# Performance work log

Measured on AMD Instinct MI355X. Metric: run time of the kernel, lower is better.

The kernel has to match this reference:

```python
import jax, jax.numpy as jnp
import numpy as np

C = 256
H = 8          # num_heads
G = 8          # groupnorm groups
EPS = 1e-6     # attention eps
GN_EPS = 1e-5  # torch GroupNorm default eps


def setup_inputs() -> dict:
    key = jax.random.key(0)
    ks = jax.random.split(key, 8)
    s = 1.0 / np.sqrt(C)
    return {
        "x": jax.random.normal(ks[0], (2, C, 32, 32, 32), dtype=jnp.float32),
        "gn_gamma": jnp.ones((C,), dtype=jnp.float32),
        "gn_beta": jnp.zeros((C,), dtype=jnp.float32),
        "wq": jax.random.normal(ks[1], (C, C), dtype=jnp.float32) * s,
        "wk": jax.random.normal(ks[2], (C, C), dtype=jnp.float32) * s,
        "wv": jax.random.normal(ks[3], (C, C), dtype=jnp.float32) * s,
        "w_out": jax.random.normal(ks[4], (C, C), dtype=jnp.float32) * s,
        "b_out": jnp.zeros((C,), dtype=jnp.float32),
    }


def reference(x, gn_gamma, gn_beta, wq, wk, wv, w_out, b_out):
    B, Cc, X, Y, Z = x.shape
    N = X * Y * Z
    D = Cc // H  # head_dim

    xf = x.reshape(B, Cc, N)

    # GroupNorm over (C/G, N) per group
    xg = xf.reshape(B, G, (Cc // G) * N)
    mean = jnp.mean(xg, axis=-1, keepdims=True)
    var = jnp.var(xg, axis=-1, keepdims=True)
    xn = ((xg - mean) * jax.lax.rsqrt(var + GN_EPS)).reshape(B, Cc, N)
    xn = xn * gn_gamma[None, :, None] + gn_beta[None, :, None]

    # 1x1x1 conv projections == channel matmuls
    q = jnp.einsum('oc,bcn->bon', wq, xn).reshape(B, H, D, N)
    k = jnp.einsum('oc,bcn->bon', wk, xn).reshape(B, H, D, N)
    v = jnp.einsum('oc,bcn->bon', wv, xn).reshape(B, H, D, N)

    qm = jax.nn.elu(q) + 1.0  # [B,H,D,N]
    km = jax.nn.elu(k) + 1.0

    # context: sum_j phi(k)_j v_j^T  -> [B,H,D,D]
    context = jnp.einsum('bhdn,bhen->bhde', km, v)
    # numerator: context @ phi(q)  -> [B,H,D,N] (axis d contracts with phi(q)'s feature dim)
    numerator = jnp.einsum('bhde,bhdn->bhen', context, qm)
    # denominator per token
    k_sum = jnp.sum(km, axis=-1)  # [B,H,D]
    denom = jnp.einsum('bhdn,bhd->bhn', qm, k_sum)  # [B,H,N]

    out = numerator / (denom[:, :, None, :] + EPS)  # [B,H,D,N]
    out = out.reshape(B, Cc, N)

    out = jnp.einsum('oc,bcn->bon', w_out, out) + b_out[None, :, None]
    out = out.reshape(B, Cc, X, Y, Z)
    return out + x
```

## Files before the change

### kernel.cpp

```cpp
#include <hip/hip_runtime.h>
#include <math.h>

#define BB 2
#define CC 256
#define NHEAD 8
#define HD 32
#define NGRP 8
#define NNTOK 32768
#define ATT_EPS 1e-6f
#define GN_EPS 1e-5f

typedef __attribute__((ext_vector_type(8))) short bfrag8;
typedef __attribute__((ext_vector_type(4))) float accf4;

__device__ __forceinline__ float b2f(unsigned short u) {
    unsigned int x = ((unsigned int)u) << 16;
    return __uint_as_float(x);
}
__device__ __forceinline__ unsigned short f2b(float f) {
    unsigned int x = __float_as_uint(f);
    unsigned int r = x + 0x7fffu + ((x >> 16) & 1u);
    return (unsigned short)(r >> 16);
}
__device__ __forceinline__ void gl_lds16(const void* g, void* s) {
    __builtin_amdgcn_global_load_lds(
        (const __attribute__((address_space(1))) unsigned int*)g,
        (__attribute__((address_space(3))) unsigned int*)s, 16, 0, 0);
}

#define WS_QMT   0ull
#define WS_XNT   (WS_QMT + 8388608ull)
#define WS_WSTOLD (WS_XNT + 8650752ull)
#define WS_PART  (WS_WSTOLD + 101632ull)
#define WS_CTX2  WS_PART
#define WS_GNP2  (WS_PART + 32768ull)
#define WS_WST2  (WS_PART + 65536ull)
#define WS_BIAS  (WS_PART + 262144ull)
#define WS_GNPO  (WS_PART + 4325376ull)
#define WS_SCALE (WS_GNPO + 2048ull)
#define WS_SHIFT (WS_SCALE + 512ull)
#define WS_CTXO  (WS_SHIFT + 512ull)
#define WS_KSUM  (WS_CTXO + 16384ull)
#define WS_AMAT  (WS_KSUM + 512ull)

#define LDS_QS_OFF  17408
#define LDS_KSP_OFF 27648
#define LDS_BIAS_OFF 49152
#define LDS_QKV_TOTAL 49664

__global__ __launch_bounds__(256) void xn_gn(const float* __restrict__ x,
                                             unsigned short* __restrict__ xn_t,
                                             float* __restrict__ gnp2) {
    __shared__ unsigned short xt[64][264];
    __shared__ float ls[64];
    int b = blockIdx.y, n0 = blockIdx.x * 64, t = threadIdx.x;
    int col4 = (t & 15) * 4;
    float gs[8], gs2[8];
    #pragma unroll
    for (int g = 0; g < 8; ++g) { gs[g] = 0.f; gs2[g] = 0.f; }
    #pragma unroll
    for (int i = 0; i < 16; ++i) {
        int c = (t >> 4) + i * 16;
        const float4 v = *(const float4*)(x + (size_t)(b * CC + c) * NNTOK + n0 + col4);
        gs[i >> 1]  += v.x + v.y + v.z + v.w;
        gs2[i >> 1] += v.x * v.x + v.y * v.y + v.z * v.z + v.w * v.w;
        xt[col4 + 0][c] = f2b(v.x);
        xt[col4 + 1][c] = f2b(v.y);
        xt[col4 + 2][c] = f2b(v.z);
        xt[col4 + 3][c] = f2b(v.w);
    }
    int lane = t & 63, w = t >> 6;
    #pragma unroll
    for (int g = 0; g < 8; ++g) {
        float a = gs[g], a2 = gs2[g];
        #pragma unroll
        for (int off = 32; off; off >>= 1) {
            a  += __shfl_down(a, off);
            a2 += __shfl_down(a2, off);
        }
        if (lane == 0) { ls[w * 16 + g * 2] = a; ls[w * 16 + g * 2 + 1] = a2; }
    }
    __syncthreads();
    if (t < 16)
        gnp2[(size_t)(b * 512 + blockIdx.x) * 16 + t] =
            ls[t] + ls[16 + t] + ls[32 + t] + ls[48 + t];
    int n = t >> 2, q = t & 3;
    const char* src = (const char*)&xt[n][0] + q * 128;
    char* dst = (char*)(xn_t + ((size_t)b * NNTOK + n0 + n) * 264) + q * 128;
    #pragma unroll
    for (int i = 0; i < 8; ++i)
        *(float4*)(dst + i * 16) = *(const float4*)(src + i * 16);
}

__global__ __launch_bounds__(256) void gn_stats2(const float* __restrict__ gnp2,
                                                 const float* __restrict__ gamma,
                                                 const float* __restrict__ beta,
                                                 float* __restrict__ scale,
                                                 float* __restrict__ shift,
                                                 float* __restrict__ ctx2) {
    __shared__ float red[256];
    __shared__ float mean_l[16], rstd_l[16];
    int t = threadIdx.x;
    for (int i = t; i < 16 * 1056; i += 256) ctx2[i] = 0.f;
    int combo = t >> 3, sl = t & 7;
    int b2 = combo >> 4, idx = combo & 15;
    float a = 0.f;
    for (int k = sl; k < 512; k += 8)
        a += gnp2[(size_t)(b2 * 512 + k) * 16 + idx];
    red[t] = a;
    __syncthreads();
    if (t < 32) {
        float s = 0.f;
        #pragma unroll
        for (int j = 0; j < 8; ++j) s += red[t * 8 + j];
        red[t] = s;
    }
    __syncthreads();
    if (t < 16) {
        const float inv = 1.0f / (float)((CC / NGRP) * NNTOK);
        float m = red[t * 2] * inv;
        float var = red[t * 2 + 1] * inv - m * m;
        mean_l[t] = m;
        rstd_l[t] = rsqrtf(var + GN_EPS);
    }
    __syncthreads();
    for (int i = t; i < BB * CC; i += 256) {
        int b = i >> 8, c = i & 255;
        int g = b * 8 + (c >> 5);
        float sc = gamma[c] * rstd_l[g];
        scale[i] = sc;
        shift[i] = beta[c] - mean_l[g] * sc;
    }
}

__global__ __launch_bounds__(256) void fold_w(const float* __restrict__ wq,
                                              const float* __restrict__ wk,
                                              const float* __restrict__ wv,
                                              const float* __restrict__ scale,
                                              const float* __restrict__ shift,
                                              unsigned short* __restrict__ Wst2,
                                              float* __restrict__ bias) {
    int slice = blockIdx.x, h = blockIdx.y, b2 = blockIdx.z, t = threadIdx.x;
    __shared__ float sc_l[256], sh_l[256];
    sc_l[t] = scale[b2 * CC + t];
    sh_l[t] = shift[b2 * CC + t];
    __syncthreads();
    const float* Ws[3] = {wq, wk, wv};
    unsigned short* wdst = Wst2 + (size_t)(b2 * NHEAD + h) * 24576;
    for (int i = slice * 3072 + t; i < (slice + 1) * 3072; i += 256) {
        int e = i & 7;
        int chunk = i >> 3;
        int lane = chunk & 63;
        int kcmi = chunk >> 6;
        int mi = kcmi % 6;
        int kc = kcmi / 6;
        int lr = lane & 15, lq = lane >> 4;
        int row = mi * 16 + lr;
        int col = kc * 32 + lq * 8 + e;
        float v = Ws[row >> 5][(size_t)(h * 32 + (row & 31)) * CC + col] * sc_l[col];
        wdst[i] = f2b(v);
    }
    if (t < 96) {
        int rl = t >> 3, sub = t & 7;
        int r = slice * 12 + rl;
        const float* wrow = Ws[r >> 5] + (size_t)(h * 32 + (r & 31)) * CC + sub * 32;
        float sp = 0.f;
        #pragma unroll
        for (int k = 0; k < 8; ++k) {
            const float4 v4 = *(const float4*)(wrow + k * 4);
            const float* shp = &sh_l[sub * 32 + k * 4];
            sp += v4.x * shp[0] + v4.y * shp[1] + v4.z * shp[2] + v4.w * shp[3];
        }
        sp += __shfl_xor(sp, 1);
        sp += __shfl_xor(sp, 2);
        sp += __shfl_xor(sp, 4);
        if (sub == 0) bias[(size_t)(b2 * NHEAD + h) * 96 + r] = sp;
    }
}

__global__ __launch_bounds__(256, 3) void qkv_ctx(
    const unsigned short* __restrict__ xn_t, const unsigned short* __restrict__ Wst2,
    const float* __restrict__ bias,
    unsigned short* __restrict__ qm_t, float* __restrict__ ctx2) {
    __shared__ char lds[LDS_QKV_TOTAL];
    const int id = blockIdx.x;
    const int xcd = id & 7;
    const int j = id >> 3;
    const int h = j & 7;
    const int rem = j >> 3;
    const int tile = xcd * 32 + (rem & 31);
    const int b = rem >> 5;
    const int t = threadIdx.x;
    const int lane = t & 63, w = t >> 6;
    const int lr = lane & 15, lq = lane >> 4;
    const int n0 = tile * 128;

    {
        const char* wg = (const char*)(Wst2 + (size_t)(b * NHEAD + h) * 24576);
        for (int jj = w; jj < 48; jj += 4)
            gl_lds16(wg + jj * 1024 + lane * 16, lds + jj * 1024);
        if (t < 96)
            ((float*)(lds + LDS_BIAS_OFF))[t] = bias[(size_t)(b * NHEAD + h) * 96 + t];
    }
    __syncthreads();

    accf4 acc[6][2];
    #pragma unroll
    for (int i = 0; i < 6; ++i)
        #pragma unroll
        for (int jj = 0; jj < 2; ++jj) acc[i][jj] = (accf4){0.f, 0.f, 0.f, 0.f};

    const unsigned short* xr0 = xn_t + ((size_t)b * NNTOK + n0 + w * 32 + lr) * 264 + lq * 8;
    const unsigned short* xr1 = xr0 + 16 * 264;
    const char* wl = lds;

    bfrag8 wnx[6], bnx[2];
    #pragma unroll
    for (int mi = 0; mi < 6; ++mi)
        wnx[mi] = *(const bfrag8*)(wl + (0 * 6 + mi) * 1024 + lane * 16);
    bnx[0] = *(const bfrag8*)xr0;
    bnx[1] = *(const bfrag8*)xr1;

    #pragma unroll
    for (int kc = 0; kc < 8; ++kc) {
        bfrag8 wcur[6];
        #pragma unroll
        for (int mi = 0; mi < 6; ++mi) wcur[mi] = wnx[mi];
        bfrag8 bcur[2] = {bnx[0], bnx[1]};
        if (kc < 7) {
            #pragma unroll
            for (int mi = 0; mi < 6; ++mi)
                wnx[mi] = *(const bfrag8*)(wl + ((kc + 1) * 6 + mi) * 1024 + lane * 16);
            bnx[0] = *(const bfrag8*)(xr0 + (kc + 1) * 32);
            bnx[1] = *(const bfrag8*)(xr1 + (kc + 1) * 32);
        }
        #pragma unroll
        for (int mi = 0; mi < 6; ++mi)
            #pragma unroll
            for (int ci = 0; ci < 2; ++ci)
                acc[mi][ci] = __builtin_amdgcn_mfma_f32_16x16x32_bf16(wcur[mi], bcur[ci], acc[mi][ci], 0, 0, 0);
    }
    __syncthreads();

    const float* biasl = (const float*)(lds + LDS_BIAS_OFF);
    char* kmv = lds;
    char* qs  = lds + LDS_QS_OFF;
    #pragma unroll
    for (int mi = 0; mi < 2; ++mi)
        #pragma unroll
        for (int ci = 0; ci < 2; ++ci)
            #pragma unroll
            for (int r = 0; r < 4; ++r) {
                int d = mi * 16 + lq * 4 + r;
                int n = w * 32 + ci * 16 + lr;
                float q = acc[mi][ci][r] + biasl[d];
                *(unsigned short*)(qs + n * 80 + d * 2) = f2b(q > 0.f ? q + 1.f : __expf(q));
            }
    #pragma unroll
    for (int mi = 2; mi < 4; ++mi)
        #pragma unroll
        for (int ci = 0; ci < 2; ++ci)
            #pragma unroll
            for (int r = 0; r < 4; ++r) {
                int d = (mi - 2) * 16 + lq * 4 + r;
                int n = w * 32 + ci * 16 + lr;
                float kk = acc[mi][ci][r] + biasl[32 + d];
                *(unsigned short*)(kmv + d * 272 + n * 2) = f2b(kk > 0.f ? kk + 1.f : __expf(kk));
            }
    #pragma unroll
    for (int mi = 4; mi < 6; ++mi)
        #pragma unroll
        for (int ci = 0; ci < 2; ++ci)
            #pragma unroll
            for (int r = 0; r < 4; ++r) {
                int e = (mi - 4) * 16 + lq * 4 + r;
                int n = w * 32 + ci * 16 + lr;
                *(unsigned short*)(kmv + (32 + e) * 272 + n * 2) = f2b(acc[mi][ci][r] + biasl[64 + e]);
            }
    __syncthreads();

    float* ctx2p = ctx2 + (size_t)(b * NHEAD + h) * 1056;

    {
        char* qg = (char*)(qm_t + ((size_t)(b * NHEAD + h) * NNTOK + n0) * 32);
        int n = t >> 1, half = t & 1;
        const char* src = qs + n * 80 + half * 32;
        char* dst = qg + n * 64 + half * 32;
        *(float4*)dst = *(const float4*)src;
        *(float4*)(dst + 16) = *(const float4*)(src + 16);
    }

    {
        int qr = w >> 1, qc = w & 1;
        accf4 cacc = (accf4){0.f, 0.f, 0.f, 0.f};
        #pragma unroll
        for (int kk = 0; kk < 4; ++kk) {
            bfrag8 a  = *(const bfrag8*)(kmv + (qr * 16 + lr) * 272 + kk * 64 + lq * 16);
            bfrag8 bb = *(const bfrag8*)(kmv + (32 + qc * 16 + lr) * 272 + kk * 64 + lq * 16);
            cacc = __builtin_amdgcn_mfma_f32_16x16x32_bf16(a, bb, cacc, 0, 0, 0);
        }
        #pragma unroll
        for (int r = 0; r < 4; ++r) {
            int d = qr * 16 + lq * 4 + r, e = qc * 16 + lr;
            atomicAdd(ctx2p + d * 32 + e, cacc[r]);
        }
    }

    {
        float* ksp = (float*)(lds + LDS_KSP_OFF);
        int d = t >> 3, oc = t & 7;
        float s = 0.f;
        for (int i = 0; i < 16; ++i)
            s += b2f(*(const unsigned short*)(kmv + d * 272 + (oc * 16 + i) * 2));
        ksp[d * 8 + oc] = s;
        __syncthreads();
        if (t < 32) {
            float s2 = 0.f;
            #pragma unroll
            for (int i = 0; i < 8; ++i) s2 += ksp[t * 8 + i];
            atomicAdd(ctx2p + 1024 + t, s2);
        }
    }
}

__global__ __launch_bounds__(256) void build_A(const float* __restrict__ w_out,
                                               const float* __restrict__ ctx2,
                                               unsigned short* __restrict__ Amat,
                                               float* __restrict__ ksum_g) {
    int ot = blockIdx.x, b = blockIdx.y, t = threadIdx.x;
    __shared__ float cs[NHEAD * HD * HD];
    for (int i = t; i < NHEAD * HD * HD; i += 256) {
        int hh = i >> 10, de = i & 1023;
        cs[i] = ctx2[(size_t)(b * NHEAD + hh) * 1056 + de];
    }
    if (ot == 0)
        ksum_g[b * CC + t] = ctx2[(size_t)(b * NHEAD + (t >> 5)) * 1056 + 1024 + (t & 31)];
    __syncthreads();
    int h = t >> 5, d = t & 31;
    for (int oi = 0; oi < 32; ++oi) {
        int o = ot * 32 + oi;
        const float* wrow = w_out + (size_t)o * CC + h * HD;
        float s = 0.f;
        #pragma unroll
        for (int e = 0; e < HD; ++e) s += wrow[e] * cs[h * 1024 + d * 32 + e];
        Amat[((size_t)(b * CC + o)) * CC + t] = f2b(s);
    }
}

#define LDSF_A   0
#define LDSF_Q   10240
#define LDSF_BO  20480
#define LDSF_KS  20992
#define LDSF_TOT 22016
__global__ __launch_bounds__(256, 4) void final_out(
    const unsigned short* __restrict__ qm_t, const unsigned short* __restrict__ Amat,
    const float* __restrict__ ksum_g, const float* __restrict__ b_out,
    const float* __restrict__ x, float* __restrict__ out) {
    __shared__ char L[LDSF_TOT];
    int tile = blockIdx.x, mt = blockIdx.y, b = blockIdx.z;
    int n0 = tile * 128, t = threadIdx.x;
    int lane = t & 63, w = t >> 6, lr = lane & 15, lq = lane >> 4;
    int wm = (w >> 1) * 64, wn = (w & 1) * 64;
    accf4 acc[4][4];
    #pragma unroll
    for (int i = 0; i < 4; ++i)
        #pragma unroll
        for (int j = 0; j < 4; ++j) acc[i][j] = (accf4){0.f, 0.f, 0.f, 0.f};

    if (t < 128) ((float*)(L + LDSF_BO))[t] = b_out[mt * 128 + t];
    ((float*)(L + LDSF_KS))[t] = ksum_g[b * CC + t];

    char* Al = L + LDSF_A;
    char* Ql = L + LDSF_Q;
    const int m = t >> 1, half = t & 1;
    const char* ag = (const char*)(Amat + (size_t)(b * CC + mt * 128 + m) * CC) + half * 32;
    const char* qg = (const char*)(qm_t + ((size_t)b * NHEAD * NNTOK + (size_t)(n0 + m)) * 32) + half * 32;

    bfrag8 a0 = *(const bfrag8*)ag;
    bfrag8 a1 = *(const bfrag8*)(ag + 16);
    bfrag8 q0 = *(const bfrag8*)qg;
    bfrag8 q1 = *(const bfrag8*)(qg + 16);

    __syncthreads();

    for (int h = 0; h < NHEAD; ++h) {
        const float* ks = (const float*)(L + LDSF_KS) + h * 32 + half * 16;
        float sp = 0.f;
        #pragma unroll
        for (int e = 0; e < 8; ++e) {
            sp += b2f((unsigned short)q0[e]) * ks[e];
            sp += b2f((unsigned short)q1[e]) * ks[8 + e];
        }
        float dot = sp + __shfl_xor(sp, 1);
        float dn = 1.0f / (dot + ATT_EPS);

        __syncthreads();
        *(bfrag8*)(Al + m * 80 + half * 32) = a0;
        *(bfrag8*)(Al + m * 80 + half * 32 + 16) = a1;
        bfrag8 s0, s1;
        #pragma unroll
        for (int e = 0; e < 8; ++e) {
            s0[e] = (short)f2b(b2f((unsigned short)q0[e]) * dn);
            s1[e] = (short)f2b(b2f((unsigned short)q1[e]) * dn);
        }
        *(bfrag8*)(Ql + m * 80 + half * 32) = s0;
        *(bfrag8*)(Ql + m * 80 + half * 32 + 16) = s1;
        __syncthreads();

        if (h < 7) {
            a0 = *(const bfrag8*)(ag + (h + 1) * 64);
            a1 = *(const bfrag8*)(ag + (h + 1) * 64 + 16);
            q0 = *(const bfrag8*)(qg + (size_t)(h + 1) * NNTOK * 64);
            q1 = *(const bfrag8*)(qg + (size_t)(h + 1) * NNTOK * 64 + 16);
        }

        bfrag8 bfr[4];
        #pragma unroll
        for (int ci = 0; ci < 4; ++ci) {
            int n = wn + ci * 16 + lr;
            bfr[ci] = *(const bfrag8*)(Ql + n * 80 + lq * 16);
        }
        #pragma unroll
        for (int mi = 0; mi < 4; ++mi) {
            bfrag8 a = *(const bfrag8*)(Al + (wm + mi * 16 + lr) * 80 + lq * 16);
            #pragma unroll
            for (int ci = 0; ci < 4; ++ci)
                acc[mi][ci] = __builtin_amdgcn_mfma_f32_16x16x32_bf16(a, bfr[ci], acc[mi][ci], 0, 0, 0);
        }
    }

    const float* bo_s = (const float*)(L + LDSF_BO);
    #pragma unroll
    for (int mi = 0; mi < 4; ++mi)
        #pragma unroll
        for (int ci = 0; ci < 4; ++ci)
            #pragma unroll
            for (int r = 0; r < 4; ++r) {
                int ol = wm + mi * 16 + lq * 4 + r;
                int n = wn + ci * 16 + lr;
                size_t idx = ((size_t)(b * CC + mt * 128 + ol)) * NNTOK + n0 + n;
                out[idx] = acc[mi][ci][r] + bo_s[ol] + x[idx];
            }
}

extern "C" void kernel_launch(void* const* d_in, const int* in_sizes, int n_in,
                              void* d_out, int out_size, void* d_ws, size_t ws_size,
                              hipStream_t stream) {
    (void)in_sizes; (void)n_in; (void)out_size; (void)ws_size;
    const float* x      = (const float*)d_in[0];
    const float* gamma  = (const float*)d_in[1];
    const float* beta   = (const float*)d_in[2];
    const float* wq     = (const float*)d_in[3];
    const float* wk     = (const float*)d_in[4];
    const float* wv     = (const float*)d_in[5];
    const float* w_out  = (const float*)d_in[6];
    const float* b_out  = (const float*)d_in[7];
    float* out = (float*)d_out;
    float* ws  = (float*)d_ws;

    unsigned short* qm_t = (unsigned short*)(ws + WS_QMT);
    unsigned short* xn_t = (unsigned short*)(ws + WS_XNT);
    float* ctx2 = ws + WS_CTX2;
    float* gnp2 = ws + WS_GNP2;
    unsigned short* Wst2 = (unsigned short*)(ws + WS_WST2);
    float* bias = ws + WS_BIAS;
    float* scale = ws + WS_SCALE;
    float* shift = ws + WS_SHIFT;
    float* ksum = ws + WS_KSUM;
    unsigned short* Amat = (unsigned short*)(ws + WS_AMAT);

    hipLaunchKernelGGL(xn_gn, dim3(NNTOK / 64, BB), dim3(256), 0, stream, x, xn_t, gnp2);
    hipLaunchKernelGGL(gn_stats2, dim3(1), dim3(256), 0, stream, gnp2, gamma, beta,
                       scale, shift, ctx2);
    hipLaunchKernelGGL(fold_w, dim3(8, 8, 2), dim3(256), 0, stream, wq, wk, wv,
                       scale, shift, Wst2, bias);
    hipLaunchKernelGGL(qkv_ctx, dim3(NNTOK / 128 * NHEAD * BB), dim3(256), 0, stream,
                       xn_t, Wst2, bias, qm_t, ctx2);
    hipLaunchKernelGGL(build_A, dim3(8, BB), dim3(256), 0, stream, w_out, ctx2, Amat, ksum);
    hipLaunchKernelGGL(final_out, dim3(NNTOK / 128, 2, BB), dim3(256), 0, stream,
                       qm_t, Amat, ksum, b_out, x, out);
}
```

Measured before the change: 244.4 us.

## Privatize context atomics per XCD, rework xn_gn loads, merge final_out M tiles

Context accumulation in qkv_ctx now targets one of eight per-XCD copies, which build_A sums, to cut atomic contention on a single buffer. The xn_gn kernel switches to coalesced per-lane scalar loads that pack eight channels into one vector LDS store, and it writes group partials directly without the LDS reduction. final_out becomes a 512-thread block that covers all 256 output channels per token tile, so the q/denominator staging is done once instead of twice. This raises LDS use, register pressure and zero-init traffic.

```diff
diff --git a/kernel.cpp b/kernel.cpp
--- a/kernel.cpp
+++ b/kernel.cpp
@@ -33,9 +33,9 @@
 #define WS_WSTOLD (WS_XNT + 8650752ull)
 #define WS_PART  (WS_WSTOLD + 101632ull)
 #define WS_CTX2  WS_PART
-#define WS_GNP2  (WS_PART + 32768ull)
-#define WS_WST2  (WS_PART + 65536ull)
-#define WS_BIAS  (WS_PART + 262144ull)
+#define WS_GNP2  (WS_PART + 135168ull)
+#define WS_WST2  (WS_PART + 151552ull)
+#define WS_BIAS  (WS_PART + 348160ull)
 #define WS_GNPO  (WS_PART + 4325376ull)
 #define WS_SCALE (WS_GNPO + 2048ull)
 #define WS_SHIFT (WS_SCALE + 512ull)
@@ -52,38 +52,34 @@
                                              unsigned short* __restrict__ xn_t,
                                              float* __restrict__ gnp2) {
     __shared__ unsigned short xt[64][264];
-    __shared__ float ls[64];
     int b = blockIdx.y, n0 = blockIdx.x * 64, t = threadIdx.x;
-    int col4 = (t & 15) * 4;
-    float gs[8], gs2[8];
-    #pragma unroll
-    for (int g = 0; g < 8; ++g) { gs[g] = 0.f; gs2[g] = 0.f; }
-    #pragma unroll
-    for (int i = 0; i < 16; ++i) {
-        int c = (t >> 4) + i * 16;
-        const float4 v = *(const float4*)(x + (size_t)(b * CC + c) * NNTOK + n0 + col4);
-        gs[i >> 1]  += v.x + v.y + v.z + v.w;
-        gs2[i >> 1] += v.x * v.x + v.y * v.y + v.z * v.z + v.w * v.w;
-        xt[col4 + 0][c] = f2b(v.x);
-        xt[col4 + 1][c] = f2b(v.y);
-        xt[col4 + 2][c] = f2b(v.z);
-        xt[col4 + 3][c] = f2b(v.w);
-    }
     int lane = t & 63, w = t >> 6;
-    #pragma unroll
-    for (int g = 0; g < 8; ++g) {
-        float a = gs[g], a2 = gs2[g];
-        #pragma unroll
-        for (int off = 32; off; off >>= 1) {
-            a  += __shfl_down(a, off);
-            a2 += __shfl_down(a2, off);
-        }
-        if (lane == 0) { ls[w * 16 + g * 2] = a; ls[w * 16 + g * 2 + 1] = a2; }
-    }
-    __syncthreads();
-    if (t < 16)
-        gnp2[(size_t)(b * 512 + blockIdx.x) * 16 + t] =
-            ls[t] + ls[16 + t] + ls[32 + t] + ls[48 + t];
+    float gs0 = 0.f, gs20 = 0.f, gs1 = 0.f, gs21 = 0.f;
+    #pragma unroll
+    for (int i = 0; i < 8; ++i) {
+        int c0 = w * 64 + i * 8;
+        bfrag8 pk;
+        float as = 0.f, as2 = 0.f;
+        #pragma unroll
+        for (int k = 0; k < 8; ++k) {
+            float v = x[(size_t)(b * CC + c0 + k) * NNTOK + n0 + lane];
+            pk[k] = (short)f2b(v);
+            as += v; as2 += v * v;
+        }
+        if (i < 4) { gs0 += as; gs20 += as2; } else { gs1 += as; gs21 += as2; }
+        *(bfrag8*)((char*)&xt[0][0] + lane * 528 + w * 128 + i * 16) = pk;
+    }
+    #pragma unroll
+    for (int off = 32; off; off >>= 1) {
+        gs0 += __shfl_down(gs0, off); gs20 += __shfl_down(gs20, off);
+        gs1 += __shfl_down(gs1, off); gs21 += __shfl_down(gs21, off);
+    }
+    if (lane == 0) {
+        float* gp = gnp2 + (size_t)(b * 512 + blockIdx.x) * 16;
+        gp[(2 * w) * 2]     = gs0;  gp[(2 * w) * 2 + 1]     = gs20;
+        gp[(2 * w + 1) * 2] = gs1;  gp[(2 * w + 1) * 2 + 1] = gs21;
+    }
+    __syncthreads();
     int n = t >> 2, q = t & 3;
     const char* src = (const char*)&xt[n][0] + q * 128;
     char* dst = (char*)(xn_t + ((size_t)b * NNTOK + n0 + n) * 264) + q * 128;
@@ -101,7 +97,8 @@
     __shared__ float red[256];
     __shared__ float mean_l[16], rstd_l[16];
     int t = threadIdx.x;
-    for (int i = t; i < 16 * 1056; i += 256) ctx2[i] = 0.f;
+    for (int i4 = t; i4 < 8 * 16 * 1056 / 4; i4 += 256)
+        *(float4*)(ctx2 + i4 * 4) = (float4){0.f, 0.f, 0.f, 0.f};
     int combo = t >> 3, sl = t & 7;
     int b2 = combo >> 4, idx = combo & 15;
     float a = 0.f;
@@ -279,7 +276,7 @@
             }
     __syncthreads();
 
-    float* ctx2p = ctx2 + (size_t)(b * NHEAD + h) * 1056;
+    float* ctx2p = ctx2 + ((size_t)(xcd * 16) + b * NHEAD + h) * 1056;
 
     {
         char* qg = (char*)(qm_t + ((size_t)(b * NHEAD + h) * NNTOK + n0) * 32);
@@ -331,10 +328,19 @@
     __shared__ float cs[NHEAD * HD * HD];
     for (int i = t; i < NHEAD * HD * HD; i += 256) {
         int hh = i >> 10, de = i & 1023;
-        cs[i] = ctx2[(size_t)(b * NHEAD + hh) * 1056 + de];
-    }
-    if (ot == 0)
-        ksum_g[b * CC + t] = ctx2[(size_t)(b * NHEAD + (t >> 5)) * 1056 + 1024 + (t & 31)];
+        float s = 0.f;
+        #pragma unroll
+        for (int xc = 0; xc < 8; ++xc)
+            s += ctx2[((size_t)(xc * 16) + b * NHEAD + hh) * 1056 + de];
+        cs[i] = s;
+    }
+    if (ot == 0) {
+        float s = 0.f;
+        #pragma unroll
+        for (int xc = 0; xc < 8; ++xc)
+            s += ctx2[((size_t)(xc * 16) + b * NHEAD + (t >> 5)) * 1056 + 1024 + (t & 31)];
+        ksum_g[b * CC + t] = s;
+    }
     __syncthreads();
     int h = t >> 5, d = t & 31;
     for (int oi = 0; oi < 32; ++oi) {
@@ -348,16 +354,16 @@
 }
 
 #define LDSF_A   0
-#define LDSF_Q   10240
-#define LDSF_BO  20480
-#define LDSF_KS  20992
-#define LDSF_TOT 22016
-__global__ __launch_bounds__(256, 4) void final_out(
+#define LDSF_Q   20480
+#define LDSF_BO  30720
+#define LDSF_KS  31744
+#define LDSF_TOT 32768
+__global__ __launch_bounds__(512, 4) void final_out(
     const unsigned short* __restrict__ qm_t, const unsigned short* __restrict__ Amat,
     const float* __restrict__ ksum_g, const float* __restrict__ b_out,
     const float* __restrict__ x, float* __restrict__ out) {
     __shared__ char L[LDSF_TOT];
-    int tile = blockIdx.x, mt = blockIdx.y, b = blockIdx.z;
+    int tile = blockIdx.x, b = blockIdx.z;
     int n0 = tile * 128, t = threadIdx.x;
     int lane = t & 63, w = t >> 6, lr = lane & 15, lq = lane >> 4;
     int wm = (w >> 1) * 64, wn = (w & 1) * 64;
@@ -367,51 +373,48 @@
         #pragma unroll
         for (int j = 0; j < 4; ++j) acc[i][j] = (accf4){0.f, 0.f, 0.f, 0.f};
 
-    if (t < 128) ((float*)(L + LDSF_BO))[t] = b_out[mt * 128 + t];
-    ((float*)(L + LDSF_KS))[t] = ksum_g[b * CC + t];
+    if (t < 256) {
+        ((float*)(L + LDSF_BO))[t] = b_out[t];
+        ((float*)(L + LDSF_KS))[t] = ksum_g[b * CC + t];
+    }
 
     char* Al = L + LDSF_A;
     char* Ql = L + LDSF_Q;
-    const int m = t >> 1, half = t & 1;
-    const char* ag = (const char*)(Amat + (size_t)(b * CC + mt * 128 + m) * CC) + half * 32;
-    const char* qg = (const char*)(qm_t + ((size_t)b * NHEAD * NNTOK + (size_t)(n0 + m)) * 32) + half * 32;
+    const int m2 = t >> 1, halfA = t & 1;
+    const char* ag = (const char*)(Amat + (size_t)(b * CC + m2) * CC) + halfA * 32;
+    const int nq = t >> 2, q4 = t & 3;
+    const char* qg = (const char*)(qm_t + ((size_t)b * NHEAD * NNTOK + (size_t)(n0 + nq)) * 32) + q4 * 16;
 
     bfrag8 a0 = *(const bfrag8*)ag;
     bfrag8 a1 = *(const bfrag8*)(ag + 16);
     bfrag8 q0 = *(const bfrag8*)qg;
-    bfrag8 q1 = *(const bfrag8*)(qg + 16);
 
     __syncthreads();
 
     for (int h = 0; h < NHEAD; ++h) {
-        const float* ks = (const float*)(L + LDSF_KS) + h * 32 + half * 16;
+        const float* ks = (const float*)(L + LDSF_KS) + h * 32 + q4 * 8;
         float sp = 0.f;
         #pragma unroll
-        for (int e = 0; e < 8; ++e) {
+        for (int e = 0; e < 8; ++e)
             sp += b2f((unsigned short)q0[e]) * ks[e];
-            sp += b2f((unsigned short)q1[e]) * ks[8 + e];
-        }
-        float dot = sp + __shfl_xor(sp, 1);
-        float dn = 1.0f / (dot + ATT_EPS);
+        sp += __shfl_xor(sp, 1);
+        sp += __shfl_xor(sp, 2);
+        float dn = 1.0f / (sp + ATT_EPS);
 
         __syncthreads();
-        *(bfrag8*)(Al + m * 80 + half * 32) = a0;
-        *(bfrag8*)(Al + m * 80 + half * 32 + 16) = a1;
-        bfrag8 s0, s1;
-        #pragma unroll
-        for (int e = 0; e < 8; ++e) {
+        *(bfrag8*)(Al + m2 * 80 + halfA * 32) = a0;
+        *(bfrag8*)(Al + m2 * 80 + halfA * 32 + 16) = a1;
+        bfrag8 s0;
+        #pragma unroll
+        for (int e = 0; e < 8; ++e)
             s0[e] = (short)f2b(b2f((unsigned short)q0[e]) * dn);
-            s1[e] = (short)f2b(b2f((unsigned short)q1[e]) * dn);
-        }
-        *(bfrag8*)(Ql + m * 80 + half * 32) = s0;
-        *(bfrag8*)(Ql + m * 80 + half * 32 + 16) = s1;
+        *(bfrag8*)(Ql + nq * 80 + q4 * 16) = s0;
         __syncthreads();
 
         if (h < 7) {
             a0 = *(const bfrag8*)(ag + (h + 1) * 64);
             a1 = *(const bfrag8*)(ag + (h + 1) * 64 + 16);
             q0 = *(const bfrag8*)(qg + (size_t)(h + 1) * NNTOK * 64);
-            q1 = *(const bfrag8*)(qg + (size_t)(h + 1) * NNTOK * 64 + 16);
         }
 
         bfrag8 bfr[4];
@@ -438,7 +441,7 @@
             for (int r = 0; r < 4; ++r) {
                 int ol = wm + mi * 16 + lq * 4 + r;
                 int n = wn + ci * 16 + lr;
-                size_t idx = ((size_t)(b * CC + mt * 128 + ol)) * NNTOK + n0 + n;
+                size_t idx = ((size_t)(b * CC + ol)) * NNTOK + n0 + n;
                 out[idx] = acc[mi][ci][r] + bo_s[ol] + x[idx];
             }
 }
@@ -477,6 +480,6 @@
     hipLaunchKernelGGL(qkv_ctx, dim3(NNTOK / 128 * NHEAD * BB), dim3(256), 0, stream,
                        xn_t, Wst2, bias, qm_t, ctx2);
     hipLaunchKernelGGL(build_A, dim3(8, BB), dim3(256), 0, stream, w_out, ctx2, Amat, ksum);
-    hipLaunchKernelGGL(final_out, dim3(NNTOK / 128, 2, BB), dim3(256), 0, stream,
+    hipLaunchKernelGGL(final_out, dim3(NNTOK / 128, 1, BB), dim3(512), 0, stream,
                        qm_t, Amat, ksum, b_out, x, out);
 }
```

After: 284.8 us. 1.17x slower.
